# Kernel tuning notes

Hardware: AMD Instinct MI355X
Metric: run time of the kernel (lower is better)

Reference implementation:

```python
import jax, jax.numpy as jnp
import numpy as np

N_NODES = 50000
N_EDGES = 800000
IN_F = 128
H_F = 128
OUT_F = 128
N_GRAPHS = 128


def setup_inputs() -> dict:
    key = jax.random.key(0)
    ks = jax.random.split(key, 7)
    x = jax.random.normal(ks[0], (N_NODES, IN_F), dtype=jnp.float32)
    edge_index = jax.random.randint(ks[1], (2, N_EDGES), 0, N_NODES, dtype=jnp.int32)
    batch = jnp.sort(jax.random.randint(ks[2], (N_NODES,), 0, N_GRAPHS, dtype=jnp.int32))
    s1 = 1.0 / np.sqrt(IN_F)
    s2 = 1.0 / np.sqrt(H_F)
    W1 = jax.random.uniform(ks[3], (IN_F, H_F), jnp.float32, -s1, s1)
    b1 = jnp.zeros((H_F,), jnp.float32)
    W2 = jax.random.uniform(ks[4], (H_F, OUT_F), jnp.float32, -s2, s2)
    b2 = jnp.zeros((OUT_F,), jnp.float32)
    return {"x": x, "edge_index": edge_index, "batch": batch,
            "W1": W1, "b1": b1, "W2": W2, "b2": b2}


def _gcn_conv(x, W, b, src, dst, n_nodes):
    # PyG GCNConv: out = D^{-1/2} (A + I) D^{-1/2} (x W) + b
    h = x @ W  # [N, out]
    # degree including self-loop
    deg = jax.ops.segment_sum(jnp.ones_like(dst, dtype=h.dtype), dst,
                              num_segments=n_nodes) + 1.0
    dinv = jax.lax.rsqrt(deg)  # [N]
    norm = dinv[src] * dinv[dst]  # [E]
    agg = jax.ops.segment_sum(h[src] * norm[:, None], dst, num_segments=n_nodes)
    # self-loop term has norm dinv[i]^2
    return agg + (dinv * dinv)[:, None] * h + b


def reference(x, edge_index, batch, W1, b1, W2, b2):
    src, dst = edge_index[0], edge_index[1]
    h = jax.nn.relu(_gcn_conv(x, W1, b1, src, dst, N_NODES))
    h = _gcn_conv(h, W2, b2, src, dst, N_NODES)
    # global_add_pool over graphs
    return jax.ops.segment_sum(h, batch, num_segments=N_GRAPHS)
```

## Files before the change

### kernel.cpp

```cpp
#include <hip/hip_runtime.h>
#include <hip/hip_bf16.h>


typedef _Float16 f16x8 __attribute__((ext_vector_type(8)));
typedef float f32x4 __attribute__((ext_vector_type(4)));

#define BCHUNK 4096

__global__ __launch_bounds__(256) void bin_hist(const int* __restrict__ ei,
                                                const float* __restrict__ W1,
                                                _Float16* __restrict__ wfrag,
                                                float* __restrict__ P,
                                                _Float16* __restrict__ hb,
                                                _Float16* __restrict__ ob,
                                                int* __restrict__ counts,
                                                int E, int N, int NB, int NBLK) {
    __shared__ int hist[256];
    int t = threadIdx.x, blk = blockIdx.x;
    int gtid = blk * 256 + t;
    int gstride = gridDim.x * 256;

    for (int i = gtid; i < 128 * 128; i += gstride) P[i] = 0.f;
    if (gtid < 64) {
        ((unsigned int*)(hb + (size_t)N * 128))[gtid] = 0u;
        ((unsigned int*)(ob + (size_t)N * 128))[gtid] = 0u;
    }
    if (gtid < 2048) {
        int lane = gtid & 63, kc = (gtid >> 6) & 3, nb = gtid >> 8;
        int col = nb * 16 + (lane & 15);
        int krow = kc * 32 + (lane >> 4) * 8;
#pragma unroll
        for (int j = 0; j < 8; j++)
            wfrag[gtid * 8 + j] = (_Float16)W1[(krow + j) * 128 + col];
    }

    for (int b = t; b < NB; b += 256) hist[b] = 0;
    __syncthreads();
    int base = blk * BCHUNK;
    int end = min(E, base + BCHUNK);
    for (int e = base + t; e < end; e += 256)
        atomicAdd(&hist[ei[E + e] >> 8], 1);
    __syncthreads();
    for (int b = t; b < NB; b += 256) counts[b * NBLK + blk] = hist[b];
}

__global__ __launch_bounds__(256) void scan_counts_seg(int* __restrict__ counts,
                                                       int* __restrict__ btot,
                                                       int NBLK, int BCAP) {
    __shared__ int s[256];
    int b = blockIdx.x, t = threadIdx.x;
    int carry = 0;
    for (int base = 0; base < NBLK; base += 256) {
        int idx = base + t;
        int v = (idx < NBLK) ? counts[b * NBLK + idx] : 0;
        s[t] = v;
        __syncthreads();
        for (int off = 1; off < 256; off *= 2) {
            int u = (t >= off) ? s[t - off] : 0;
            __syncthreads();
            s[t] += u;
            __syncthreads();
        }
        int excl = s[t] - v + carry;
        if (idx < NBLK) counts[b * NBLK + idx] = b * BCAP + excl;
        carry += s[255];
        __syncthreads();
    }
    if (t == 0) btot[b] = carry;
}

__global__ __launch_bounds__(256) void bin_scatter(const int* __restrict__ ei,
                                                   const int* __restrict__ counts,
                                                   unsigned int* __restrict__ bedges,
                                                   int E, int NB, int NBLK) {
    __shared__ int lcur[256];
    int t = threadIdx.x, blk = blockIdx.x;
    for (int b = t; b < NB; b += 256) lcur[b] = counts[b * NBLK + blk];
    __syncthreads();
    int base = blk * BCHUNK;
    int end = min(E, base + BCHUNK);
    for (int e = base + t; e < end; e += 256) {
        int s = ei[e];
        int d = ei[E + e];
        int pos = atomicAdd(&lcur[d >> 8], 1);
        bedges[pos] = (unsigned int)s | ((unsigned int)(d & 255) << 16);
    }
}

__global__ __launch_bounds__(256) void build_csr(const unsigned int* __restrict__ bedges,
                                                 const int* __restrict__ btot,
                                                 int* __restrict__ cnt,
                                                 int* __restrict__ row_start,
                                                 float* __restrict__ dinv,
                                                 int* __restrict__ srcs,
                                                 int N, int BCAP, int SCAP) {
    __shared__ int lcnt[256];
    __shared__ int lpre[256];
    __shared__ int lcur[256];
    int b = blockIdx.x, t = threadIdx.x;
    int node = (b << 8) + t;
    lcnt[t] = 0;
    __syncthreads();
    int bstart = b * BCAP;
    int bend = bstart + btot[b];
    for (int i = bstart + t; i < bend; i += 256)
        atomicAdd(&lcnt[bedges[i] >> 16], 1);
    __syncthreads();
    int c = lcnt[t];
    int pc = (c + 7) & ~7;
    lpre[t] = pc;
    __syncthreads();
    for (int off = 1; off < 256; off *= 2) {
        int u = (t >= off) ? lpre[t - off] : 0;
        __syncthreads();
        lpre[t] += u;
        __syncthreads();
    }
    int rs = b * SCAP + lpre[t] - pc;
    if (node < N) {
        row_start[node] = rs;
        cnt[node] = c;
        dinv[node] = rsqrtf((float)c + 1.0f);
    }
    lcur[t] = rs;
    __syncthreads();
    for (int i = bstart + t; i < bend; i += 256) {
        unsigned int p = bedges[i];
        int pos = atomicAdd(&lcur[p >> 16], 1);
        srcs[pos] = (int)(p & 0xffffu);
    }
    if (node < N) {
        for (int j = rs + c; j < rs + pc; j++) srcs[j] = N;
    }
}

__global__ __launch_bounds__(256) void gemm_mfma_f32in(const float* __restrict__ A,
                                                       const _Float16* __restrict__ wfrag,
                                                       const float* __restrict__ dinv,
                                                       _Float16* __restrict__ C, int M) {
    __shared__ _Float16 As[128 * 136];
    int t = threadIdx.x;
    int row0 = blockIdx.x * 128;

    const float4* A4 = (const float4*)A;
#pragma unroll
    for (int it = 0; it < 16; it++) {
        int v = it * 256 + t;
        int row = v >> 5;
        int seg = v & 31;
        float4 val = make_float4(0.f, 0.f, 0.f, 0.f);
        if (row0 + row < M) val = A4[(size_t)(row0 + row) * 32 + seg];
        _Float16* pp = &As[row * 136 + seg * 4];
        pp[0] = (_Float16)val.x; pp[1] = (_Float16)val.y;
        pp[2] = (_Float16)val.z; pp[3] = (_Float16)val.w;
    }
    __syncthreads();

    int wv = t >> 6;
    int lane = t & 63;
    int lrow = lane & 15;
    int lq = lane >> 4;

    f32x4 acc[2][8];
#pragma unroll
    for (int i = 0; i < 2; i++)
#pragma unroll
        for (int j = 0; j < 8; j++) acc[i][j] = (f32x4){0.f, 0.f, 0.f, 0.f};

#pragma unroll
    for (int kc = 0; kc < 4; kc++) {
        int k0 = kc * 32;
        f16x8 a0 = *((const f16x8*)&As[(wv * 32 + lrow) * 136 + k0 + lq * 8]);
        f16x8 a1 = *((const f16x8*)&As[(wv * 32 + 16 + lrow) * 136 + k0 + lq * 8]);
#pragma unroll
        for (int nb = 0; nb < 8; nb++) {
            f16x8 b = ((const f16x8*)wfrag)[(nb * 4 + kc) * 64 + lane];
            acc[0][nb] = __builtin_amdgcn_mfma_f32_16x16x32_f16(a0, b, acc[0][nb], 0, 0, 0);
            acc[1][nb] = __builtin_amdgcn_mfma_f32_16x16x32_f16(a1, b, acc[1][nb], 0, 0, 0);
        }
    }

#pragma unroll
    for (int ti = 0; ti < 2; ti++) {
#pragma unroll
        for (int r = 0; r < 4; r++) {
            int row = row0 + wv * 32 + ti * 16 + lq * 4 + r;
            if (row < M) {
                float dv = dinv[row];
#pragma unroll
                for (int nb = 0; nb < 8; nb++)
                    C[(size_t)row * 128 + nb * 16 + lrow] = (_Float16)(acc[ti][nb][r] * dv);
            }
        }
    }
}

__global__ __launch_bounds__(256) void agg1(const _Float16* __restrict__ hb,
                                            const int* __restrict__ srcs,
                                            const int* __restrict__ row_start,
                                            const int* __restrict__ cnt,
                                            const float* __restrict__ dinv,
                                            const float* __restrict__ bias,
                                            _Float16* __restrict__ ob, int n) {
    int node = blockIdx.x * 4 + (threadIdx.x >> 6);
    if (node >= n) return;
    int lane = threadIdx.x & 63;
    int cc = lane & 15;
    int sg = lane >> 4;
    int s0 = row_start[node];
    int c = cnt[node];
    int nit = (c + 7) >> 3;
    float dn = dinv[node];

    float acc[8];
#pragma unroll
    for (int j = 0; j < 8; j++) acc[j] = 0.f;

    const int* sp = srcs + s0;
    int i0 = 0, i1 = 0;
    if (nit > 0) { i0 = sp[sg]; i1 = sp[4 + sg]; }
    for (int it = 0; it < nit; it++) {
        int cs0 = i0, cs1 = i1;
        int nxt = (it + 1 < nit) ? (it + 1) : it;
        i0 = sp[nxt * 8 + sg]; i1 = sp[nxt * 8 + 4 + sg];
        f16x8 v0 = *((const f16x8*)&hb[(size_t)(unsigned)cs0 * 128 + cc * 8]);
        f16x8 v1 = *((const f16x8*)&hb[(size_t)(unsigned)cs1 * 128 + cc * 8]);
#pragma unroll
        for (int j = 0; j < 8; j++) acc[j] += (float)v0[j];
#pragma unroll
        for (int j = 0; j < 8; j++) acc[j] += (float)v1[j];
    }
#pragma unroll
    for (int j = 0; j < 8; j++) {
        acc[j] += __shfl_xor(acc[j], 16);
        acc[j] += __shfl_xor(acc[j], 32);
    }
    f16x8 hs = *((const f16x8*)&hb[(size_t)node * 128 + cc * 8]);
    float4 b0 = ((const float4*)bias)[cc * 2];
    float4 b1v = ((const float4*)bias)[cc * 2 + 1];
    float bb[8] = {b0.x, b0.y, b0.z, b0.w, b1v.x, b1v.y, b1v.z, b1v.w};
    f16x8 o;
#pragma unroll
    for (int j = 0; j < 8; j++) {
        float tv = acc[j] + (float)hs[j];
        tv = fmaxf(fmaf(dn, tv, bb[j]), 0.f) * dn;
        o[j] = (_Float16)tv;
    }
    if (sg == 0) *((f16x8*)&ob[(size_t)node * 128 + cc * 8]) = o;
}

__global__ __launch_bounds__(256) void agg2_pool(const _Float16* __restrict__ ob,
                                                 const int* __restrict__ srcs,
                                                 const int* __restrict__ row_start,
                                                 const int* __restrict__ cnt,
                                                 const float* __restrict__ dinv,
                                                 const int* __restrict__ batch,
                                                 float* __restrict__ P, int n) {
    __shared__ float red[4][128];
    int wv = threadIdx.x >> 6;
    int lane = threadIdx.x & 63;
    int cc = lane & 15;
    int sg = lane >> 4;
    int base = blockIdx.x * 4;
    int node = base + wv;

    float t8[8];
#pragma unroll
    for (int j = 0; j < 8; j++) t8[j] = 0.f;
    int g = -1;

    if (node < n) {
        g = batch[node];
        int s0 = row_start[node];
        int c = cnt[node];
        int nit = (c + 7) >> 3;
        float dn = dinv[node];

        float acc[8];
#pragma unroll
        for (int j = 0; j < 8; j++) acc[j] = 0.f;
        const int* sp = srcs + s0;
        int i0 = 0, i1 = 0;
        if (nit > 0) { i0 = sp[sg]; i1 = sp[4 + sg]; }
        for (int it = 0; it < nit; it++) {
            int cs0 = i0, cs1 = i1;
            int nxt = (it + 1 < nit) ? (it + 1) : it;
            i0 = sp[nxt * 8 + sg]; i1 = sp[nxt * 8 + 4 + sg];
            f16x8 v0 = *((const f16x8*)&ob[(size_t)(unsigned)cs0 * 128 + cc * 8]);
            f16x8 v1 = *((const f16x8*)&ob[(size_t)(unsigned)cs1 * 128 + cc * 8]);
#pragma unroll
            for (int j = 0; j < 8; j++) acc[j] += (float)v0[j];
#pragma unroll
            for (int j = 0; j < 8; j++) acc[j] += (float)v1[j];
        }
#pragma unroll
        for (int j = 0; j < 8; j++) {
            acc[j] += __shfl_xor(acc[j], 16);
            acc[j] += __shfl_xor(acc[j], 32);
        }
        f16x8 hs = *((const f16x8*)&ob[(size_t)node * 128 + cc * 8]);
#pragma unroll
        for (int j = 0; j < 8; j++) t8[j] = dn * (acc[j] + (float)hs[j]);
    }

    int lastn = min(base + 3, n - 1);
    bool uniform = (base < n) && (batch[base] == batch[lastn]) && (base + 3 < n);
    if (uniform) {
        if (sg == 0) {
#pragma unroll
            for (int j = 0; j < 8; j++) red[wv][cc * 8 + j] = t8[j];
        }
        __syncthreads();
        if (wv == 0) {
            int col = lane * 2;
            float sx = red[0][col] + red[1][col] + red[2][col] + red[3][col];
            float sy = red[0][col + 1] + red[1][col + 1] + red[2][col + 1] + red[3][col + 1];
            atomicAdd(&P[g * 128 + col], sx);
            atomicAdd(&P[g * 128 + col + 1], sy);
        }
    } else if (node < n) {
        if (sg == 0) {
#pragma unroll
            for (int j = 0; j < 8; j++) atomicAdd(&P[g * 128 + cc * 8 + j], t8[j]);
        }
    }
}

__global__ __launch_bounds__(128) void gemm_small(const float* __restrict__ P,
                                                  const float* __restrict__ W2,
                                                  const float* __restrict__ b2,
                                                  const int* __restrict__ batch,
                                                  float* __restrict__ out, int n) {
    __shared__ float prow[128];
    int g = blockIdx.x;
    int c = threadIdx.x;
    prow[c] = P[g * 128 + c];
    __syncthreads();
    int lo = 0, hi = n;
    while (lo < hi) { int mid = (lo + hi) >> 1; if (batch[mid] < g) lo = mid + 1; else hi = mid; }
    int start = lo;
    hi = n;
    while (lo < hi) { int mid = (lo + hi) >> 1; if (batch[mid] < g + 1) lo = mid + 1; else hi = mid; }
    float ng = (float)(lo - start);
    float acc = 0.f;
#pragma unroll 8
    for (int k = 0; k < 128; k++) acc = fmaf(prow[k], W2[k * 128 + c], acc);
    out[g * 128 + c] = acc + ng * b2[c];
}

extern "C" void kernel_launch(void* const* d_in, const int* in_sizes, int n_in,
                              void* d_out, int out_size, void* d_ws, size_t ws_size,
                              hipStream_t stream) {
    const float* x  = (const float*)d_in[0];
    const int*   ei = (const int*)d_in[1];
    const int*   batch = (const int*)d_in[2];
    const float* W1 = (const float*)d_in[3];
    const float* b1 = (const float*)d_in[4];
    const float* W2 = (const float*)d_in[5];
    const float* b2 = (const float*)d_in[6];
    float* out = (float*)d_out;

    const int N = in_sizes[2];
    const int E = in_sizes[1] / 2;
    const int G = out_size / 128;

    const int NB = (N + 255) >> 8;
    const int NBLK = (E + BCHUNK - 1) / BCHUNK;
    const int ncounts = NB * NBLK;
    const int BCAP = 8192;
    const int SCAP = BCAP + 2048;

    _Float16* hb = (_Float16*)d_ws;
    _Float16* ob = hb + (size_t)(N + 8) * 128;
    int* cnt  = (int*)(ob + (size_t)(N + 8) * 128);
    int* row_start = cnt + N;
    float* dinv    = (float*)(row_start + N);
    int* srcs      = (int*)(dinv + N);
    unsigned int* bedges = (unsigned int*)(srcs + (size_t)NB * SCAP);
    int* counts    = (int*)(bedges + (size_t)NB * BCAP);
    int* btot      = counts + ncounts;
    _Float16* wfrag1 = (_Float16*)(btot + NB);
    float* P       = (float*)(wfrag1 + 128 * 128);

    bin_hist<<<NBLK, 256, 0, stream>>>(ei, W1, wfrag1, P, hb, ob, counts, E, N, NB, NBLK);
    scan_counts_seg<<<NB, 256, 0, stream>>>(counts, btot, NBLK, BCAP);
    bin_scatter<<<NBLK, 256, 0, stream>>>(ei, counts, bedges, E, NB, NBLK);
    build_csr<<<NB, 256, 0, stream>>>(bedges, btot, cnt, row_start, dinv, srcs, N, BCAP, SCAP);

    gemm_mfma_f32in<<<(N + 127) / 128, 256, 0, stream>>>(x, wfrag1, dinv, hb, N);
    agg1<<<(N + 3) / 4, 256, 0, stream>>>(hb, srcs, row_start, cnt, dinv, b1, ob, N);
    agg2_pool<<<(N + 3) / 4, 256, 0, stream>>>(ob, srcs, row_start, cnt, dinv, batch, P, N);
    gemm_small<<<G, 128, 0, stream>>>(P, W2, b2, batch, out, N);
}
```

Measured before the change: 217.6 us.

## Split node features into XCD-pinned column slices for aggregation kernels

The hidden feature buffers are re-laid out as four 32-column slices, each holding all nodes contiguously. Aggregation blocks are mapped so each pair of XCDs (chosen by blockIdx modulo 8) always gathers from one slice, with each block handling 128 nodes. The aim is to keep each XCD's gather working set small enough to stay in its local L2 instead of streaming whole rows. In exchange each gather is only 8 bytes per lane, and every node's neighbour list is walked four times, once per slice. Pooling now accumulates per graph across a block's nodes and flushes with atomics only when the graph changes.

```diff
diff --git a/kernel.cpp b/kernel.cpp
--- a/kernel.cpp
+++ b/kernel.cpp
@@ -6,6 +6,21 @@
 typedef float f32x4 __attribute__((ext_vector_type(4)));
 
 #define BCHUNK 4096
+#define NPB 128
+
+static __device__ __forceinline__ float f16lo(unsigned int u) {
+    union { unsigned short s; _Float16 h; } c; c.s = (unsigned short)(u & 0xffff);
+    return (float)c.h;
+}
+static __device__ __forceinline__ float f16hi(unsigned int u) {
+    union { unsigned short s; _Float16 h; } c; c.s = (unsigned short)(u >> 16);
+    return (float)c.h;
+}
+static __device__ __forceinline__ unsigned int pack2f16(float x, float y) {
+    union { unsigned short s; _Float16 h; } a, b;
+    a.h = (_Float16)x; b.h = (_Float16)y;
+    return (unsigned int)a.s | ((unsigned int)b.s << 16);
+}
 
 __global__ __launch_bounds__(256) void bin_hist(const int* __restrict__ ei,
                                                 const float* __restrict__ W1,
@@ -19,11 +34,13 @@
     int t = threadIdx.x, blk = blockIdx.x;
     int gtid = blk * 256 + t;
     int gstride = gridDim.x * 256;
+    int NP8 = N + 8;
 
     for (int i = gtid; i < 128 * 128; i += gstride) P[i] = 0.f;
     if (gtid < 64) {
-        ((unsigned int*)(hb + (size_t)N * 128))[gtid] = 0u;
-        ((unsigned int*)(ob + (size_t)N * 128))[gtid] = 0u;
+        int s = gtid >> 4, j = gtid & 15;
+        ((unsigned int*)hb)[(size_t)s * NP8 * 16 + (size_t)N * 16 + j] = 0u;
+        ((unsigned int*)ob)[(size_t)s * NP8 * 16 + (size_t)N * 16 + j] = 0u;
     }
     if (gtid < 2048) {
         int lane = gtid & 63, kc = (gtid >> 6) & 3, nb = gtid >> 8;
@@ -137,7 +154,8 @@
 __global__ __launch_bounds__(256) void gemm_mfma_f32in(const float* __restrict__ A,
                                                        const _Float16* __restrict__ wfrag,
                                                        const float* __restrict__ dinv,
-                                                       _Float16* __restrict__ C, int M) {
+                                                       _Float16* __restrict__ C,
+                                                       int M, int NP8) {
     __shared__ _Float16 As[128 * 136];
     int t = threadIdx.x;
     int row0 = blockIdx.x * 128;
@@ -188,8 +206,11 @@
             if (row < M) {
                 float dv = dinv[row];
 #pragma unroll
-                for (int nb = 0; nb < 8; nb++)
-                    C[(size_t)row * 128 + nb * 16 + lrow] = (_Float16)(acc[ti][nb][r] * dv);
+                for (int nb = 0; nb < 8; nb++) {
+                    int slice = nb >> 1;
+                    C[(size_t)slice * NP8 * 32 + (size_t)row * 32 + (nb & 1) * 16 + lrow] =
+                        (_Float16)(acc[ti][nb][r] * dv);
+                }
             }
         }
     }
@@ -201,52 +222,53 @@
                                             const int* __restrict__ cnt,
                                             const float* __restrict__ dinv,
                                             const float* __restrict__ bias,
-                                            _Float16* __restrict__ ob, int n) {
-    int node = blockIdx.x * 4 + (threadIdx.x >> 6);
-    if (node >= n) return;
-    int lane = threadIdx.x & 63;
-    int cc = lane & 15;
-    int sg = lane >> 4;
-    int s0 = row_start[node];
-    int c = cnt[node];
-    int nit = (c + 7) >> 3;
-    float dn = dinv[node];
-
-    float acc[8];
-#pragma unroll
-    for (int j = 0; j < 8; j++) acc[j] = 0.f;
-
-    const int* sp = srcs + s0;
-    int i0 = 0, i1 = 0;
-    if (nit > 0) { i0 = sp[sg]; i1 = sp[4 + sg]; }
-    for (int it = 0; it < nit; it++) {
-        int cs0 = i0, cs1 = i1;
-        int nxt = (it + 1 < nit) ? (it + 1) : it;
-        i0 = sp[nxt * 8 + sg]; i1 = sp[nxt * 8 + 4 + sg];
-        f16x8 v0 = *((const f16x8*)&hb[(size_t)(unsigned)cs0 * 128 + cc * 8]);
-        f16x8 v1 = *((const f16x8*)&hb[(size_t)(unsigned)cs1 * 128 + cc * 8]);
-#pragma unroll
-        for (int j = 0; j < 8; j++) acc[j] += (float)v0[j];
-#pragma unroll
-        for (int j = 0; j < 8; j++) acc[j] += (float)v1[j];
-    }
-#pragma unroll
-    for (int j = 0; j < 8; j++) {
-        acc[j] += __shfl_xor(acc[j], 16);
-        acc[j] += __shfl_xor(acc[j], 32);
-    }
-    f16x8 hs = *((const f16x8*)&hb[(size_t)node * 128 + cc * 8]);
-    float4 b0 = ((const float4*)bias)[cc * 2];
-    float4 b1v = ((const float4*)bias)[cc * 2 + 1];
-    float bb[8] = {b0.x, b0.y, b0.z, b0.w, b1v.x, b1v.y, b1v.z, b1v.w};
-    f16x8 o;
-#pragma unroll
-    for (int j = 0; j < 8; j++) {
-        float tv = acc[j] + (float)hs[j];
-        tv = fmaxf(fmaf(dn, tv, bb[j]), 0.f) * dn;
-        o[j] = (_Float16)tv;
-    }
-    if (sg == 0) *((f16x8*)&ob[(size_t)node * 128 + cc * 8]) = o;
+                                            _Float16* __restrict__ ob,
+                                            int n, int NBLKS, int NP8) {
+    int xcd = blockIdx.x & 7;
+    int slice = xcd >> 1;
+    int nb = (blockIdx.x >> 3) * 2 + (xcd & 1);
+    if (nb >= NBLKS) return;
+    int wv = threadIdx.x >> 6, lane = threadIdx.x & 63;
+    int eg = lane >> 3, c8 = lane & 7;
+    const uint2* h2 = (const uint2*)hb + (size_t)slice * NP8 * 8;
+    uint2* obs = (uint2*)ob + (size_t)slice * NP8 * 8;
+    float4 bv = ((const float4*)bias)[slice * 8 + c8];
+    int base = nb * NPB;
+    for (int i = wv; i < NPB; i += 4) {
+        int node = base + i;
+        if (node >= n) break;
+        int s0 = row_start[node];
+        int c = cnt[node];
+        int nit = (c + 7) >> 3;
+        float dn = dinv[node];
+        const int* sp = srcs + s0;
+        float a0 = 0.f, a1 = 0.f, a2 = 0.f, a3 = 0.f;
+        int spre = (nit > 0) ? sp[eg] : 0;
+        for (int it = 0; it < nit; it++) {
+            int scur = spre;
+            int nxt = (it + 1 < nit) ? it + 1 : it;
+            spre = sp[nxt * 8 + eg];
+            uint2 v = h2[(size_t)(unsigned)scur * 8 + c8];
+            a0 += f16lo(v.x); a1 += f16hi(v.x);
+            a2 += f16lo(v.y); a3 += f16hi(v.y);
+        }
+#pragma unroll
+        for (int off = 8; off <= 32; off <<= 1) {
+            a0 += __shfl_xor(a0, off); a1 += __shfl_xor(a1, off);
+            a2 += __shfl_xor(a2, off); a3 += __shfl_xor(a3, off);
+        }
+        uint2 hs = h2[(size_t)node * 8 + c8];
+        float o0 = fmaxf(fmaf(dn, a0 + f16lo(hs.x), bv.x), 0.f) * dn;
+        float o1 = fmaxf(fmaf(dn, a1 + f16hi(hs.x), bv.y), 0.f) * dn;
+        float o2 = fmaxf(fmaf(dn, a2 + f16lo(hs.y), bv.z), 0.f) * dn;
+        float o3 = fmaxf(fmaf(dn, a3 + f16hi(hs.y), bv.w), 0.f) * dn;
+        if (eg == 0) {
+            uint2 w;
+            w.x = pack2f16(o0, o1);
+            w.y = pack2f16(o2, o3);
+            obs[(size_t)node * 8 + c8] = w;
+        }
+    }
 }
 
 __global__ __launch_bounds__(256) void agg2_pool(const _Float16* __restrict__ ob,
@@ -255,74 +277,64 @@
                                                  const int* __restrict__ cnt,
                                                  const float* __restrict__ dinv,
                                                  const int* __restrict__ batch,
-                                                 float* __restrict__ P, int n) {
-    __shared__ float red[4][128];
-    int wv = threadIdx.x >> 6;
-    int lane = threadIdx.x & 63;
-    int cc = lane & 15;
-    int sg = lane >> 4;
-    int base = blockIdx.x * 4;
-    int node = base + wv;
-
-    float t8[8];
-#pragma unroll
-    for (int j = 0; j < 8; j++) t8[j] = 0.f;
-    int g = -1;
-
-    if (node < n) {
-        g = batch[node];
+                                                 float* __restrict__ P,
+                                                 int n, int NBLKS, int NP8) {
+    int xcd = blockIdx.x & 7;
+    int slice = xcd >> 1;
+    int nb = (blockIdx.x >> 3) * 2 + (xcd & 1);
+    if (nb >= NBLKS) return;
+    int wv = threadIdx.x >> 6, lane = threadIdx.x & 63;
+    int eg = lane >> 3, c8 = lane & 7;
+    const uint2* h2 = (const uint2*)ob + (size_t)slice * NP8 * 8;
+    int colb = slice * 32 + c8 * 4;
+    int base = nb * NPB;
+    float p0 = 0.f, p1 = 0.f, p2 = 0.f, p3 = 0.f;
+    int gcur = -1;
+    for (int i = wv; i < NPB; i += 4) {
+        int node = base + i;
+        if (node >= n) break;
+        int g = batch[node];
+        if (g != gcur) {
+            if (gcur >= 0 && eg == 0) {
+                atomicAdd(&P[gcur * 128 + colb + 0], p0);
+                atomicAdd(&P[gcur * 128 + colb + 1], p1);
+                atomicAdd(&P[gcur * 128 + colb + 2], p2);
+                atomicAdd(&P[gcur * 128 + colb + 3], p3);
+            }
+            gcur = g;
+            p0 = p1 = p2 = p3 = 0.f;
+        }
         int s0 = row_start[node];
         int c = cnt[node];
         int nit = (c + 7) >> 3;
         float dn = dinv[node];
-
-        float acc[8];
-#pragma unroll
-        for (int j = 0; j < 8; j++) acc[j] = 0.f;
         const int* sp = srcs + s0;
-        int i0 = 0, i1 = 0;
-        if (nit > 0) { i0 = sp[sg]; i1 = sp[4 + sg]; }
+        float a0 = 0.f, a1 = 0.f, a2 = 0.f, a3 = 0.f;
+        int spre = (nit > 0) ? sp[eg] : 0;
         for (int it = 0; it < nit; it++) {
-            int cs0 = i0, cs1 = i1;
-            int nxt = (it + 1 < nit) ? (it + 1) : it;
-            i0 = sp[nxt * 8 + sg]; i1 = sp[nxt * 8 + 4 + sg];
-            f16x8 v0 = *((const f16x8*)&ob[(size_t)(unsigned)cs0 * 128 + cc * 8]);
-            f16x8 v1 = *((const f16x8*)&ob[(size_t)(unsigned)cs1 * 128 + cc * 8]);
-#pragma unroll
-            for (int j = 0; j < 8; j++) acc[j] += (float)v0[j];
-#pragma unroll
-            for (int j = 0; j < 8; j++) acc[j] += (float)v1[j];
-        }
-#pragma unroll
-        for (int j = 0; j < 8; j++) {
-            acc[j] += __shfl_xor(acc[j], 16);
-            acc[j] += __shfl_xor(acc[j], 32);
-        }
-        f16x8 hs = *((const f16x8*)&ob[(size_t)node * 128 + cc * 8]);
-#pragma unroll
-        for (int j = 0; j < 8; j++) t8[j] = dn * (acc[j] + (float)hs[j]);
-    }
-
-    int lastn = min(base + 3, n - 1);
-    bool uniform = (base < n) && (batch[base] == batch[lastn]) && (base + 3 < n);
-    if (uniform) {
-        if (sg == 0) {
-#pragma unroll
-            for (int j = 0; j < 8; j++) red[wv][cc * 8 + j] = t8[j];
-        }
-        __syncthreads();
-        if (wv == 0) {
-            int col = lane * 2;
-            float sx = red[0][col] + red[1][col] + red[2][col] + red[3][col];
-            float sy = red[0][col + 1] + red[1][col + 1] + red[2][col + 1] + red[3][col + 1];
-            atomicAdd(&P[g * 128 + col], sx);
-            atomicAdd(&P[g * 128 + col + 1], sy);
-        }
-    } else if (node < n) {
-        if (sg == 0) {
-#pragma unroll
-            for (int j = 0; j < 8; j++) atomicAdd(&P[g * 128 + cc * 8 + j], t8[j]);
-        }
+            int scur = spre;
+            int nxt = (it + 1 < nit) ? it + 1 : it;
+            spre = sp[nxt * 8 + eg];
+            uint2 v = h2[(size_t)(unsigned)scur * 8 + c8];
+            a0 += f16lo(v.x); a1 += f16hi(v.x);
+            a2 += f16lo(v.y); a3 += f16hi(v.y);
+        }
+#pragma unroll
+        for (int off = 8; off <= 32; off <<= 1) {
+            a0 += __shfl_xor(a0, off); a1 += __shfl_xor(a1, off);
+            a2 += __shfl_xor(a2, off); a3 += __shfl_xor(a3, off);
+        }
+        uint2 hs = h2[(size_t)node * 8 + c8];
+        p0 += dn * (a0 + f16lo(hs.x));
+        p1 += dn * (a1 + f16hi(hs.x));
+        p2 += dn * (a2 + f16lo(hs.y));
+        p3 += dn * (a3 + f16hi(hs.y));
+    }
+    if (gcur >= 0 && eg == 0) {
+        atomicAdd(&P[gcur * 128 + colb + 0], p0);
+        atomicAdd(&P[gcur * 128 + colb + 1], p1);
+        atomicAdd(&P[gcur * 128 + colb + 2], p2);
+        atomicAdd(&P[gcur * 128 + colb + 3], p3);
     }
 }
 
@@ -363,6 +375,7 @@
     const int N = in_sizes[2];
     const int E = in_sizes[1] / 2;
     const int G = out_size / 128;
+    const int NP8 = N + 8;
 
     const int NB = (N + 255) >> 8;
     const int NBLK = (E + BCHUNK - 1) / BCHUNK;
@@ -371,8 +384,8 @@
     const int SCAP = BCAP + 2048;
 
     _Float16* hb = (_Float16*)d_ws;
-    _Float16* ob = hb + (size_t)(N + 8) * 128;
-    int* cnt  = (int*)(ob + (size_t)(N + 8) * 128);
+    _Float16* ob = hb + (size_t)NP8 * 128;
+    int* cnt  = (int*)(ob + (size_t)NP8 * 128);
     int* row_start = cnt + N;
     float* dinv    = (float*)(row_start + N);
     int* srcs      = (int*)(dinv + N);
@@ -382,13 +395,16 @@
     _Float16* wfrag1 = (_Float16*)(btot + NB);
     float* P       = (float*)(wfrag1 + 128 * 128);
 
+    const int NBLKS = (N + NPB - 1) / NPB;
+    const int AGRID = 8 * ((NBLKS + 1) / 2);
+
     bin_hist<<<NBLK, 256, 0, stream>>>(ei, W1, wfrag1, P, hb, ob, counts, E, N, NB, NBLK);
     scan_counts_seg<<<NB, 256, 0, stream>>>(counts, btot, NBLK, BCAP);
     bin_scatter<<<NBLK, 256, 0, stream>>>(ei, counts, bedges, E, NB, NBLK);
     build_csr<<<NB, 256, 0, stream>>>(bedges, btot, cnt, row_start, dinv, srcs, N, BCAP, SCAP);
 
-    gemm_mfma_f32in<<<(N + 127) / 128, 256, 0, stream>>>(x, wfrag1, dinv, hb, N);
-    agg1<<<(N + 3) / 4, 256, 0, stream>>>(hb, srcs, row_start, cnt, dinv, b1, ob, N);
-    agg2_pool<<<(N + 3) / 4, 256, 0, stream>>>(ob, srcs, row_start, cnt, dinv, batch, P, N);
+    gemm_mfma_f32in<<<(N + 127) / 128, 256, 0, stream>>>(x, wfrag1, dinv, hb, N, NP8);
+    agg1<<<AGRID, 256, 0, stream>>>(hb, srcs, row_start, cnt, dinv, b1, ob, N, NBLKS, NP8);
+    agg2_pool<<<AGRID, 256, 0, stream>>>(ob, srcs, row_start, cnt, dinv, batch, P, N, NBLKS, NP8);
     gemm_small<<<G, 128, 0, stream>>>(P, W2, b2, batch, out, N);
 }
```

Result: slower. 303.3 us (+39.4%).

## Process four nodes per wavefront in aggregation kernels to raise memory-level parallelism

Applied to the files above, without the earlier changes.

Each wavefront in agg1 and agg2_pool now walks the neighbor lists of four nodes at once, interleaving their gather loads so more independent row fetches are in flight. The grid shrinks to one block per 16 nodes. agg2_pool extends its block-uniform pooling check to 16 nodes and merges same-graph partial sums before issuing atomics, which cuts atomic traffic. In exchange, register pressure rises with four accumulator sets, and nodes with uneven degrees leave lanes idle while the longest list finishes.

```diff
diff --git a/kernel.cpp b/kernel.cpp
--- a/kernel.cpp
+++ b/kernel.cpp
@@ -6,6 +6,12 @@
 typedef float f32x4 __attribute__((ext_vector_type(4)));
 
 #define BCHUNK 4096
+
+static __device__ __forceinline__ unsigned int pack2f16(float x, float y) {
+    union { unsigned short s; _Float16 h; } a, b;
+    a.h = (_Float16)x; b.h = (_Float16)y;
+    return (unsigned int)a.s | ((unsigned int)b.s << 16);
+}
 
 __global__ __launch_bounds__(256) void bin_hist(const int* __restrict__ ei,
                                                 const float* __restrict__ W1,
@@ -195,6 +201,19 @@
     }
 }
 
+#define GSTEP(NIT, P0, P1, SP, ACC)                                              \
+    if (it < NIT) {                                                              \
+        int c0 = P0, c1 = P1;                                                    \
+        int nx = (it + 1 < NIT) ? it + 1 : it;                                   \
+        P0 = SP[nx * 8 + sg]; P1 = SP[nx * 8 + 4 + sg];                          \
+        f16x8 v0 = *((const f16x8*)&src_rows[(size_t)(unsigned)c0 * 128 + cc * 8]); \
+        f16x8 v1 = *((const f16x8*)&src_rows[(size_t)(unsigned)c1 * 128 + cc * 8]); \
+        _Pragma("unroll")                                                        \
+        for (int j = 0; j < 8; j++) ACC[j] += (float)v0[j];                      \
+        _Pragma("unroll")                                                        \
+        for (int j = 0; j < 8; j++) ACC[j] += (float)v1[j];                      \
+    }
+
 __global__ __launch_bounds__(256) void agg1(const _Float16* __restrict__ hb,
                                             const int* __restrict__ srcs,
                                             const int* __restrict__ row_start,
@@ -202,51 +221,81 @@
                                             const float* __restrict__ dinv,
                                             const float* __restrict__ bias,
                                             _Float16* __restrict__ ob, int n) {
-    int node = blockIdx.x * 4 + (threadIdx.x >> 6);
-    if (node >= n) return;
-    int lane = threadIdx.x & 63;
-    int cc = lane & 15;
-    int sg = lane >> 4;
-    int s0 = row_start[node];
-    int c = cnt[node];
-    int nit = (c + 7) >> 3;
-    float dn = dinv[node];
-
-    float acc[8];
-#pragma unroll
-    for (int j = 0; j < 8; j++) acc[j] = 0.f;
-
-    const int* sp = srcs + s0;
-    int i0 = 0, i1 = 0;
-    if (nit > 0) { i0 = sp[sg]; i1 = sp[4 + sg]; }
-    for (int it = 0; it < nit; it++) {
-        int cs0 = i0, cs1 = i1;
-        int nxt = (it + 1 < nit) ? (it + 1) : it;
-        i0 = sp[nxt * 8 + sg]; i1 = sp[nxt * 8 + 4 + sg];
-        f16x8 v0 = *((const f16x8*)&hb[(size_t)(unsigned)cs0 * 128 + cc * 8]);
-        f16x8 v1 = *((const f16x8*)&hb[(size_t)(unsigned)cs1 * 128 + cc * 8]);
-#pragma unroll
-        for (int j = 0; j < 8; j++) acc[j] += (float)v0[j];
-#pragma unroll
-        for (int j = 0; j < 8; j++) acc[j] += (float)v1[j];
+    int wv = threadIdx.x >> 6, lane = threadIdx.x & 63;
+    int cc = lane & 15, sg = lane >> 4;
+    int n0 = blockIdx.x * 16 + wv * 4;
+    if (n0 >= n) return;
+    const _Float16* src_rows = hb;
+
+    int nit0 = 0, nit1 = 0, nit2 = 0, nit3 = 0;
+    float dn0 = 0.f, dn1 = 0.f, dn2 = 0.f, dn3 = 0.f;
+    const int *sp0 = srcs, *sp1 = srcs, *sp2 = srcs, *sp3 = srcs;
+    bool h1 = (n0 + 1 < n), h2 = (n0 + 2 < n), h3 = (n0 + 3 < n);
+    nit0 = (cnt[n0] + 7) >> 3; dn0 = dinv[n0]; sp0 = srcs + row_start[n0];
+    if (h1) { nit1 = (cnt[n0+1] + 7) >> 3; dn1 = dinv[n0+1]; sp1 = srcs + row_start[n0+1]; }
+    if (h2) { nit2 = (cnt[n0+2] + 7) >> 3; dn2 = dinv[n0+2]; sp2 = srcs + row_start[n0+2]; }
+    if (h3) { nit3 = (cnt[n0+3] + 7) >> 3; dn3 = dinv[n0+3]; sp3 = srcs + row_start[n0+3]; }
+
+    float acc0[8], acc1[8], acc2[8], acc3[8];
+#pragma unroll
+    for (int j = 0; j < 8; j++) { acc0[j] = 0.f; acc1[j] = 0.f; acc2[j] = 0.f; acc3[j] = 0.f; }
+
+    int a0 = 0, a1 = 0, b0 = 0, b1 = 0, c0_ = 0, c1_ = 0, d0 = 0, d1 = 0;
+    if (nit0 > 0) { a0 = sp0[sg]; a1 = sp0[4 + sg]; }
+    if (nit1 > 0) { b0 = sp1[sg]; b1 = sp1[4 + sg]; }
+    if (nit2 > 0) { c0_ = sp2[sg]; c1_ = sp2[4 + sg]; }
+    if (nit3 > 0) { d0 = sp3[sg]; d1 = sp3[4 + sg]; }
+    int itmax = max(max(nit0, nit1), max(nit2, nit3));
+    for (int it = 0; it < itmax; it++) {
+        GSTEP(nit0, a0, a1, sp0, acc0)
+        GSTEP(nit1, b0, b1, sp1, acc1)
+        GSTEP(nit2, c0_, c1_, sp2, acc2)
+        GSTEP(nit3, d0, d1, sp3, acc3)
     }
 #pragma unroll
     for (int j = 0; j < 8; j++) {
-        acc[j] += __shfl_xor(acc[j], 16);
-        acc[j] += __shfl_xor(acc[j], 32);
-    }
-    f16x8 hs = *((const f16x8*)&hb[(size_t)node * 128 + cc * 8]);
-    float4 b0 = ((const float4*)bias)[cc * 2];
-    float4 b1v = ((const float4*)bias)[cc * 2 + 1];
-    float bb[8] = {b0.x, b0.y, b0.z, b0.w, b1v.x, b1v.y, b1v.z, b1v.w};
-    f16x8 o;
-#pragma unroll
-    for (int j = 0; j < 8; j++) {
-        float tv = acc[j] + (float)hs[j];
-        tv = fmaxf(fmaf(dn, tv, bb[j]), 0.f) * dn;
-        o[j] = (_Float16)tv;
-    }
-    if (sg == 0) *((f16x8*)&ob[(size_t)node * 128 + cc * 8]) = o;
+        acc0[j] += __shfl_xor(acc0[j], 16); acc0[j] += __shfl_xor(acc0[j], 32);
+        acc1[j] += __shfl_xor(acc1[j], 16); acc1[j] += __shfl_xor(acc1[j], 32);
+        acc2[j] += __shfl_xor(acc2[j], 16); acc2[j] += __shfl_xor(acc2[j], 32);
+        acc3[j] += __shfl_xor(acc3[j], 16); acc3[j] += __shfl_xor(acc3[j], 32);
+    }
+    float4 q0 = ((const float4*)bias)[cc * 2];
+    float4 q1 = ((const float4*)bias)[cc * 2 + 1];
+    float bb[8] = {q0.x, q0.y, q0.z, q0.w, q1.x, q1.y, q1.z, q1.w};
+    if (sg == 0) {
+        {
+            f16x8 hs = *((const f16x8*)&hb[(size_t)n0 * 128 + cc * 8]);
+            f16x8 o;
+#pragma unroll
+            for (int j = 0; j < 8; j++)
+                o[j] = (_Float16)(fmaxf(fmaf(dn0, acc0[j] + (float)hs[j], bb[j]), 0.f) * dn0);
+            *((f16x8*)&ob[(size_t)n0 * 128 + cc * 8]) = o;
+        }
+        if (h1) {
+            f16x8 hs = *((const f16x8*)&hb[(size_t)(n0+1) * 128 + cc * 8]);
+            f16x8 o;
+#pragma unroll
+            for (int j = 0; j < 8; j++)
+                o[j] = (_Float16)(fmaxf(fmaf(dn1, acc1[j] + (float)hs[j], bb[j]), 0.f) * dn1);
+            *((f16x8*)&ob[(size_t)(n0+1) * 128 + cc * 8]) = o;
+        }
+        if (h2) {
+            f16x8 hs = *((const f16x8*)&hb[(size_t)(n0+2) * 128 + cc * 8]);
+            f16x8 o;
+#pragma unroll
+            for (int j = 0; j < 8; j++)
+                o[j] = (_Float16)(fmaxf(fmaf(dn2, acc2[j] + (float)hs[j], bb[j]), 0.f) * dn2);
+            *((f16x8*)&ob[(size_t)(n0+2) * 128 + cc * 8]) = o;
+        }
+        if (h3) {
+            f16x8 hs = *((const f16x8*)&hb[(size_t)(n0+3) * 128 + cc * 8]);
+            f16x8 o;
+#pragma unroll
+            for (int j = 0; j < 8; j++)
+                o[j] = (_Float16)(fmaxf(fmaf(dn3, acc3[j] + (float)hs[j], bb[j]), 0.f) * dn3);
+            *((f16x8*)&ob[(size_t)(n0+3) * 128 + cc * 8]) = o;
+        }
+    }
 }
 
 __global__ __launch_bounds__(256) void agg2_pool(const _Float16* __restrict__ ob,
@@ -257,71 +306,116 @@
                                                  const int* __restrict__ batch,
                                                  float* __restrict__ P, int n) {
     __shared__ float red[4][128];
-    int wv = threadIdx.x >> 6;
-    int lane = threadIdx.x & 63;
-    int cc = lane & 15;
-    int sg = lane >> 4;
-    int base = blockIdx.x * 4;
-    int node = base + wv;
-
-    float t8[8];
-#pragma unroll
-    for (int j = 0; j < 8; j++) t8[j] = 0.f;
-    int g = -1;
-
-    if (node < n) {
-        g = batch[node];
-        int s0 = row_start[node];
-        int c = cnt[node];
-        int nit = (c + 7) >> 3;
-        float dn = dinv[node];
-
-        float acc[8];
-#pragma unroll
-        for (int j = 0; j < 8; j++) acc[j] = 0.f;
-        const int* sp = srcs + s0;
-        int i0 = 0, i1 = 0;
-        if (nit > 0) { i0 = sp[sg]; i1 = sp[4 + sg]; }
-        for (int it = 0; it < nit; it++) {
-            int cs0 = i0, cs1 = i1;
-            int nxt = (it + 1 < nit) ? (it + 1) : it;
-            i0 = sp[nxt * 8 + sg]; i1 = sp[nxt * 8 + 4 + sg];
-            f16x8 v0 = *((const f16x8*)&ob[(size_t)(unsigned)cs0 * 128 + cc * 8]);
-            f16x8 v1 = *((const f16x8*)&ob[(size_t)(unsigned)cs1 * 128 + cc * 8]);
-#pragma unroll
-            for (int j = 0; j < 8; j++) acc[j] += (float)v0[j];
-#pragma unroll
-            for (int j = 0; j < 8; j++) acc[j] += (float)v1[j];
+    int wv = threadIdx.x >> 6, lane = threadIdx.x & 63;
+    int cc = lane & 15, sg = lane >> 4;
+    int base = blockIdx.x * 16;
+    int n0 = base + wv * 4;
+    const _Float16* src_rows = ob;
+
+    float acc0[8], acc1[8], acc2[8], acc3[8];
+#pragma unroll
+    for (int j = 0; j < 8; j++) { acc0[j] = 0.f; acc1[j] = 0.f; acc2[j] = 0.f; acc3[j] = 0.f; }
+    bool h0 = (n0 < n), h1 = (n0 + 1 < n), h2 = (n0 + 2 < n), h3 = (n0 + 3 < n);
+    int g0 = -1, g1 = -1, g2 = -1, g3 = -1;
+
+    if (h0) {
+        int nit0 = (cnt[n0] + 7) >> 3;
+        float dn0 = dinv[n0];
+        const int* sp0 = srcs + row_start[n0];
+        g0 = batch[n0];
+        int nit1 = 0, nit2 = 0, nit3 = 0;
+        float dn1 = 0.f, dn2 = 0.f, dn3 = 0.f;
+        const int *sp1 = srcs, *sp2 = srcs, *sp3 = srcs;
+        if (h1) { nit1 = (cnt[n0+1] + 7) >> 3; dn1 = dinv[n0+1]; sp1 = srcs + row_start[n0+1]; g1 = batch[n0+1]; }
+        if (h2) { nit2 = (cnt[n0+2] + 7) >> 3; dn2 = dinv[n0+2]; sp2 = srcs + row_start[n0+2]; g2 = batch[n0+2]; }
+        if (h3) { nit3 = (cnt[n0+3] + 7) >> 3; dn3 = dinv[n0+3]; sp3 = srcs + row_start[n0+3]; g3 = batch[n0+3]; }
+
+        int a0 = 0, a1 = 0, b0 = 0, b1 = 0, c0_ = 0, c1_ = 0, d0 = 0, d1 = 0;
+        if (nit0 > 0) { a0 = sp0[sg]; a1 = sp0[4 + sg]; }
+        if (nit1 > 0) { b0 = sp1[sg]; b1 = sp1[4 + sg]; }
+        if (nit2 > 0) { c0_ = sp2[sg]; c1_ = sp2[4 + sg]; }
+        if (nit3 > 0) { d0 = sp3[sg]; d1 = sp3[4 + sg]; }
+        int itmax = max(max(nit0, nit1), max(nit2, nit3));
+        for (int it = 0; it < itmax; it++) {
+            GSTEP(nit0, a0, a1, sp0, acc0)
+            GSTEP(nit1, b0, b1, sp1, acc1)
+            GSTEP(nit2, c0_, c1_, sp2, acc2)
+            GSTEP(nit3, d0, d1, sp3, acc3)
         }
 #pragma unroll
         for (int j = 0; j < 8; j++) {
-            acc[j] += __shfl_xor(acc[j], 16);
-            acc[j] += __shfl_xor(acc[j], 32);
-        }
-        f16x8 hs = *((const f16x8*)&ob[(size_t)node * 128 + cc * 8]);
-#pragma unroll
-        for (int j = 0; j < 8; j++) t8[j] = dn * (acc[j] + (float)hs[j]);
-    }
-
-    int lastn = min(base + 3, n - 1);
-    bool uniform = (base < n) && (batch[base] == batch[lastn]) && (base + 3 < n);
+            acc0[j] += __shfl_xor(acc0[j], 16); acc0[j] += __shfl_xor(acc0[j], 32);
+            acc1[j] += __shfl_xor(acc1[j], 16); acc1[j] += __shfl_xor(acc1[j], 32);
+            acc2[j] += __shfl_xor(acc2[j], 16); acc2[j] += __shfl_xor(acc2[j], 32);
+            acc3[j] += __shfl_xor(acc3[j], 16); acc3[j] += __shfl_xor(acc3[j], 32);
+        }
+        {
+            f16x8 hs = *((const f16x8*)&ob[(size_t)n0 * 128 + cc * 8]);
+#pragma unroll
+            for (int j = 0; j < 8; j++) acc0[j] = dn0 * (acc0[j] + (float)hs[j]);
+        }
+        if (h1) {
+            f16x8 hs = *((const f16x8*)&ob[(size_t)(n0+1) * 128 + cc * 8]);
+#pragma unroll
+            for (int j = 0; j < 8; j++) acc1[j] = dn1 * (acc1[j] + (float)hs[j]);
+        }
+        if (h2) {
+            f16x8 hs = *((const f16x8*)&ob[(size_t)(n0+2) * 128 + cc * 8]);
+#pragma unroll
+            for (int j = 0; j < 8; j++) acc2[j] = dn2 * (acc2[j] + (float)hs[j]);
+        }
+        if (h3) {
+            f16x8 hs = *((const f16x8*)&ob[(size_t)(n0+3) * 128 + cc * 8]);
+#pragma unroll
+            for (int j = 0; j < 8; j++) acc3[j] = dn3 * (acc3[j] + (float)hs[j]);
+        }
+    }
+
+    int lastn = min(base + 15, n - 1);
+    bool uniform = (base < n) && (batch[base] == batch[lastn]) && (base + 15 < n);
     if (uniform) {
         if (sg == 0) {
 #pragma unroll
-            for (int j = 0; j < 8; j++) red[wv][cc * 8 + j] = t8[j];
+            for (int j = 0; j < 8; j++)
+                red[wv][cc * 8 + j] = acc0[j] + acc1[j] + acc2[j] + acc3[j];
         }
         __syncthreads();
         if (wv == 0) {
             int col = lane * 2;
             float sx = red[0][col] + red[1][col] + red[2][col] + red[3][col];
             float sy = red[0][col + 1] + red[1][col + 1] + red[2][col + 1] + red[3][col + 1];
-            atomicAdd(&P[g * 128 + col], sx);
-            atomicAdd(&P[g * 128 + col + 1], sy);
-        }
-    } else if (node < n) {
-        if (sg == 0) {
-#pragma unroll
-            for (int j = 0; j < 8; j++) atomicAdd(&P[g * 128 + cc * 8 + j], t8[j]);
+            atomicAdd(&P[g0 * 128 + col], sx);
+            atomicAdd(&P[g0 * 128 + col + 1], sy);
+        }
+    } else if (h0 && sg == 0) {
+        if (h1 && g1 == g0) {
+#pragma unroll
+            for (int j = 0; j < 8; j++) acc0[j] += acc1[j];
+            g1 = -1;
+        }
+        if (h3 && g3 == g2) {
+#pragma unroll
+            for (int j = 0; j < 8; j++) acc2[j] += acc3[j];
+            g3 = -1;
+        }
+        if (h2 && g2 == g0 && g1 < 0) {
+#pragma unroll
+            for (int j = 0; j < 8; j++) acc0[j] += acc2[j];
+            g2 = -1;
+        }
+#pragma unroll
+        for (int j = 0; j < 8; j++) atomicAdd(&P[g0 * 128 + cc * 8 + j], acc0[j]);
+        if (g1 >= 0) {
+#pragma unroll
+            for (int j = 0; j < 8; j++) atomicAdd(&P[g1 * 128 + cc * 8 + j], acc1[j]);
+        }
+        if (g2 >= 0 && h2) {
+#pragma unroll
+            for (int j = 0; j < 8; j++) atomicAdd(&P[g2 * 128 + cc * 8 + j], acc2[j]);
+        }
+        if (g3 >= 0 && h3) {
+#pragma unroll
+            for (int j = 0; j < 8; j++) atomicAdd(&P[g3 * 128 + cc * 8 + j], acc3[j]);
         }
     }
 }
@@ -388,7 +482,7 @@
     build_csr<<<NB, 256, 0, stream>>>(bedges, btot, cnt, row_start, dinv, srcs, N, BCAP, SCAP);
 
     gemm_mfma_f32in<<<(N + 127) / 128, 256, 0, stream>>>(x, wfrag1, dinv, hb, N);
-    agg1<<<(N + 3) / 4, 256, 0, stream>>>(hb, srcs, row_start, cnt, dinv, b1, ob, N);
-    agg2_pool<<<(N + 3) / 4, 256, 0, stream>>>(ob, srcs, row_start, cnt, dinv, batch, P, N);
+    agg1<<<(N + 15) / 16, 256, 0, stream>>>(hb, srcs, row_start, cnt, dinv, b1, ob, N);
+    agg2_pool<<<(N + 15) / 16, 256, 0, stream>>>(ob, srcs, row_start, cnt, dinv, batch, P, N);
     gemm_small<<<G, 128, 0, stream>>>(P, W2, b2, batch, out, N);
 }
```

New measurement: 224.2 us. 1.03x slower.
